# Kernel tuning notes

Hardware: AMD Instinct MI355X
Metric: run time of the kernel (lower is better)

Reference implementation:

```python
import jax, jax.numpy as jnp
import numpy as np

L_MAX = 3          # max output angular momentum (L_max in the module)
N_L_IN = 4         # input l = 0..3, all with sigma = +1
Q = 16             # q_max per input block
N_SAMPLES = 4000   # number of atomic environments (samples)


def _combos():
    # Mirrors CGIteration.initialize: for each (l1,s1=1) x (l2,s2=1) pair,
    # emit L in |l1-l2|..min(l1+l2, L_max), S = (-1)^(l1+l2+L).
    out = []
    for l1 in range(N_L_IN):
        for l2 in range(N_L_IN):
            for L in range(abs(l1 - l2), min(l1 + l2, L_MAX) + 1):
                out.append((l1, l2, L, (-1) ** (l1 + l2 + L)))
    return out


def setup_inputs() -> dict:
    key = jax.random.key(0)
    ks = jax.random.split(key, 9)
    inp = {}
    for l in range(N_L_IN):
        inp[f"x1_l{l}"] = jax.random.normal(ks[l], (N_SAMPLES, 2 * l + 1, Q), dtype=jnp.float32)
        inp[f"x2_l{l}"] = jax.random.normal(ks[4 + l], (N_SAMPLES, 2 * l + 1, Q), dtype=jnp.float32)
    # Padded Clebsch-Gordan coefficient table: cg_coeffs[l1, l2, L, m1, m2, M]
    # (slices [:2l1+1, :2l2+1, :2L+1] are used; padding is ignored).
    inp["cg_coeffs"] = jax.random.normal(
        ks[8], (N_L_IN, N_L_IN, L_MAX + 1, 2 * N_L_IN - 1, 2 * N_L_IN - 1, 2 * L_MAX + 1),
        dtype=jnp.float32)
    return inp


def _forward(x1, x2, cg_coeffs):
    # One species; per-(L,S) output block lists, then concat along properties.
    blocks = {}
    for l1, l2, L, S in _combos():
        C = cg_coeffs[l1, l2, L, :2 * l1 + 1, :2 * l2 + 1, :2 * L + 1]  # [m1, m2, M]
        # cg.combine with 'full' selected_features == full cartesian (q1, q2)
        # outer product: out[n, M, q1, q2] = sum_{m1,m2} C[m1,m2,M] x1[n,m1,q1] x2[n,m2,q2]
        b = jnp.einsum('nip,njq,ijM->nMpq', x1[l1], x2[l2], C)
        b = b.reshape(b.shape[0], 2 * L + 1, -1)  # [n, 2L+1, q1*q2]
        blocks.setdefault((L, S), []).append(b)
    outs = []
    for key in sorted(blocks.keys()):
        v = jnp.concatenate(blocks[key], axis=-1)      # cat along 'mixed' properties
        outs.append(v.reshape(v.shape[0], -1))         # flatten (m, properties)
    return jnp.concatenate(outs, axis=-1)              # [n, 39936]


def reference(x1_l0, x1_l1, x1_l2, x1_l3, x2_l0, x2_l1, x2_l2, x2_l3, cg_coeffs):
    x1 = [x1_l0, x1_l1, x1_l2, x1_l3]
    x2 = [x2_l0, x2_l1, x2_l2, x2_l3]
    return _forward(x1, x2, cg_coeffs)
```

## Files before the change

### kernel.cpp

```cpp
#include <hip/hip_runtime.h>


namespace {

constexpr int NC = 34;

struct CInfo { int l1, l2, L, pbase, outbase, mstride; };
struct CTable { CInfo c[NC]; int packed_total; int outsize; };

constexpr CTable build_table() {
  CTable t{};
  int nb[4][2] = {};
  for (int l1 = 0; l1 < 4; ++l1)
    for (int l2 = 0; l2 < 4; ++l2) {
      int lo = l1 > l2 ? l1 - l2 : l2 - l1;
      int hi = (l1 + l2 < 3) ? l1 + l2 : 3;
      for (int L = lo; L <= hi; ++L)
        nb[L][((l1 + l2 + L) & 1) ? 0 : 1]++;
    }
  int keyoff[4][2] = {};
  int off = 0;
  for (int L = 0; L < 4; ++L)
    for (int s = 0; s < 2; ++s) {
      keyoff[L][s] = off;
      off += (2 * L + 1) * 256 * nb[L][s];
    }
  t.outsize = off;
  int blk[4][2] = {};
  int idx = 0, pb = 0;
  for (int l1 = 0; l1 < 4; ++l1)
    for (int l2 = 0; l2 < 4; ++l2) {
      int lo = l1 > l2 ? l1 - l2 : l2 - l1;
      int hi = (l1 + l2 < 3) ? l1 + l2 : 3;
      for (int L = lo; L <= hi; ++L) {
        int s = ((l1 + l2 + L) & 1) ? 0 : 1;
        pb = (pb + 15) & ~15;
        t.c[idx].l1 = l1; t.c[idx].l2 = l2; t.c[idx].L = L;
        t.c[idx].pbase = pb;
        t.c[idx].outbase = keyoff[L][s] + blk[L][s] * 256;
        t.c[idx].mstride = 256 * nb[L][s];
        blk[L][s]++;
        pb += (2 * l1 + 1) * (2 * l2 + 1) * (2 * L + 1);
        ++idx;
      }
    }
  t.packed_total = pb;
  return t;
}

constexpr CTable CTAB = build_table();
static_assert(CTAB.outsize == 39936, "output layout mismatch");
static_assert(CTAB.packed_total <= 4096, "packed cg exceeds 16KB");

template <int CI>
__device__ __forceinline__ void pack_combo(const float* __restrict__ cg,
                                           float* __restrict__ cgp, int tid) {
  if constexpr (CI < NC) {
    constexpr CInfo c = CTAB.c[CI];
    constexpr int D2 = 2 * c.l2 + 1, DL = 2 * c.L + 1;
    constexpr int SZ = (2 * c.l1 + 1) * D2 * DL;
    for (int tt = tid; tt < SZ; tt += 256) {
      int M = tt % DL, ij = tt / DL;
      int j = ij % D2, i = ij / D2;
      cgp[c.pbase + tt] =
          cg[((((c.l1 * 4 + c.l2) * 4 + c.L) * 7 + i) * 7 + j) * 7 + M];
    }
    pack_combo<CI + 1>(cg, cgp, tid);
  }
}

__global__ void pack_cg_kernel(const float* __restrict__ cg,
                               float* __restrict__ cgp) {
  pack_combo<0>(cg, cgp, (int)threadIdx.x);
}

template <int CI>
__device__ __forceinline__ void run_combos(const float* __restrict__ cgp,
                                           const float (&x1r)[16],
                                           const float (&x2r)[16],
                                           float* __restrict__ outn) {
  if constexpr (CI < NC) {
    constexpr CInfo c = CTAB.c[CI];
    constexpr int D1 = 2 * c.l1 + 1, D2 = 2 * c.l2 + 1, DL = 2 * c.L + 1;
    constexpr int R1 = c.l1 * c.l1, R2 = c.l2 * c.l2;
    float acc[DL];
#pragma unroll
    for (int M = 0; M < DL; ++M) acc[M] = 0.f;
#pragma unroll
    for (int i = 0; i < D1; ++i) {
#pragma unroll
      for (int j = 0; j < D2; ++j) {
        const float ab = x1r[R1 + i] * x2r[R2 + j];
#pragma unroll
        for (int M = 0; M < DL; ++M)
          acc[M] = fmaf(cgp[c.pbase + (i * D2 + j) * DL + M], ab, acc[M]);
      }
    }
#pragma unroll
    for (int M = 0; M < DL; ++M)
      outn[c.outbase + M * c.mstride] = acc[M];
    run_combos<CI + 1>(cgp, x1r, x2r, outn);
  }
}

__global__ __launch_bounds__(256) void cg_main(
    const float* __restrict__ x1_0, const float* __restrict__ x2_0,
    const float* __restrict__ x1_1, const float* __restrict__ x2_1,
    const float* __restrict__ x1_2, const float* __restrict__ x2_2,
    const float* __restrict__ x1_3, const float* __restrict__ x2_3,
    const float* __restrict__ cgp_, float* __restrict__ out) {
  const float* cgp = (const float*)__builtin_assume_aligned(cgp_, 256);
  __shared__ float x1s[16][16];
  __shared__ float x2s[16][16];
  const int tid = (int)threadIdx.x;
  const int n = (int)blockIdx.x;
  const int r = tid >> 4, col = tid & 15;
  const float* s1; const float* s2; int ri;
  if (r < 1)      { s1 = x1_0 + n * 16;  s2 = x2_0 + n * 16;  ri = r; }
  else if (r < 4) { s1 = x1_1 + n * 48;  s2 = x2_1 + n * 48;  ri = r - 1; }
  else if (r < 9) { s1 = x1_2 + n * 80;  s2 = x2_2 + n * 80;  ri = r - 4; }
  else            { s1 = x1_3 + n * 112; s2 = x2_3 + n * 112; ri = r - 9; }
  x1s[r][col] = s1[ri * 16 + col];
  x2s[r][col] = s2[ri * 16 + col];
  __syncthreads();
  float x1r[16], x2r[16];
#pragma unroll
  for (int k = 0; k < 16; ++k) {
    x1r[k] = x1s[k][r];
    x2r[k] = x2s[k][col];
  }
  float* outn = out + (size_t)n * (size_t)CTAB.outsize + tid;
  run_combos<0>(cgp, x1r, x2r, outn);
}

}

extern "C" void kernel_launch(void* const* d_in, const int* in_sizes, int n_in,
                              void* d_out, int out_size, void* d_ws,
                              size_t ws_size, hipStream_t stream) {
  const float* x1[4];
  const float* x2[4];
  if (in_sizes[1] == in_sizes[0]) {
    for (int l = 0; l < 4; ++l) {
      x1[l] = (const float*)d_in[2 * l];
      x2[l] = (const float*)d_in[2 * l + 1];
    }
  } else {
    for (int l = 0; l < 4; ++l) {
      x1[l] = (const float*)d_in[l];
      x2[l] = (const float*)d_in[4 + l];
    }
  }
  const float* cg = (const float*)d_in[8];
  float* out = (float*)d_out;
  float* cgp = (float*)d_ws;

  const int n = in_sizes[0] / 16;

  pack_cg_kernel<<<1, 256, 0, stream>>>(cg, cgp);
  cg_main<<<n, 256, 0, stream>>>(x1[0], x2[0], x1[1], x2[1], x1[2], x2[2],
                                 x1[3], x2[3], cgp, out);
}
```

Before: 168.8 us.

## Stage output segments in LDS and write them with vectorized nontemporal stores

```diff
diff --git a/kernel.cpp b/kernel.cpp
--- a/kernel.cpp
+++ b/kernel.cpp
@@ -3,30 +3,39 @@
 
 namespace {
 
+typedef float f32x4 __attribute__((ext_vector_type(4)));
+
 constexpr int NC = 34;
-
-struct CInfo { int l1, l2, L, pbase, outbase, mstride; };
-struct CTable { CInfo c[NC]; int packed_total; int outsize; };
-
-constexpr CTable build_table() {
-  CTable t{};
-  int nb[4][2] = {};
+constexpr int SEGF = 6144;
+
+struct CInfo { int l1, l2, L, s, pbase, blk, nb, segbase; };
+struct PInfo { int kidx, M0, M1, base, floats; };
+struct Tables {
+  CInfo c[NC];
+  PInfo p[16];
+  int np;
+  int packed_total;
+  int outsize;
+};
+
+constexpr Tables build() {
+  Tables t{};
+  int nb[8] = {};
   for (int l1 = 0; l1 < 4; ++l1)
     for (int l2 = 0; l2 < 4; ++l2) {
       int lo = l1 > l2 ? l1 - l2 : l2 - l1;
       int hi = (l1 + l2 < 3) ? l1 + l2 : 3;
       for (int L = lo; L <= hi; ++L)
-        nb[L][((l1 + l2 + L) & 1) ? 0 : 1]++;
-    }
-  int keyoff[4][2] = {};
+        nb[L * 2 + (((l1 + l2 + L) & 1) ? 0 : 1)]++;
+    }
+  int segbase[8] = {};
   int off = 0;
-  for (int L = 0; L < 4; ++L)
-    for (int s = 0; s < 2; ++s) {
-      keyoff[L][s] = off;
-      off += (2 * L + 1) * 256 * nb[L][s];
-    }
+  for (int k = 0; k < 8; ++k) {
+    segbase[k] = off;
+    off += (2 * (k >> 1) + 1) * 256 * nb[k];
+  }
   t.outsize = off;
-  int blk[4][2] = {};
+  int blk[8] = {};
   int idx = 0, pb = 0;
   for (int l1 = 0; l1 < 4; ++l1)
     for (int l2 = 0; l2 < 4; ++l2) {
@@ -34,29 +43,49 @@
       int hi = (l1 + l2 < 3) ? l1 + l2 : 3;
       for (int L = lo; L <= hi; ++L) {
         int s = ((l1 + l2 + L) & 1) ? 0 : 1;
+        int k = L * 2 + s;
         pb = (pb + 15) & ~15;
-        t.c[idx].l1 = l1; t.c[idx].l2 = l2; t.c[idx].L = L;
+        t.c[idx].l1 = l1; t.c[idx].l2 = l2; t.c[idx].L = L; t.c[idx].s = s;
         t.c[idx].pbase = pb;
-        t.c[idx].outbase = keyoff[L][s] + blk[L][s] * 256;
-        t.c[idx].mstride = 256 * nb[L][s];
-        blk[L][s]++;
+        t.c[idx].blk = blk[k];
+        t.c[idx].nb = nb[k];
+        t.c[idx].segbase = segbase[k];
+        blk[k]++;
         pb += (2 * l1 + 1) * (2 * l2 + 1) * (2 * L + 1);
         ++idx;
       }
     }
   t.packed_total = pb;
+  int np = 0;
+  for (int k = 0; k < 8; ++k) {
+    if (nb[k] == 0) continue;
+    int DL = 2 * (k >> 1) + 1;
+    int sr = nb[k] * 256;
+    int maxsr = SEGF / sr;
+    int M0 = 0;
+    while (M0 < DL) {
+      int M1 = M0 + maxsr < DL ? M0 + maxsr : DL;
+      t.p[np].kidx = k; t.p[np].M0 = M0; t.p[np].M1 = M1;
+      t.p[np].base = segbase[k] + M0 * sr;
+      t.p[np].floats = (M1 - M0) * sr;
+      ++np;
+      M0 = M1;
+    }
+  }
+  t.np = np;
   return t;
 }
 
-constexpr CTable CTAB = build_table();
-static_assert(CTAB.outsize == 39936, "output layout mismatch");
-static_assert(CTAB.packed_total <= 4096, "packed cg exceeds 16KB");
+constexpr Tables TAB = build();
+static_assert(TAB.outsize == 39936, "output layout mismatch");
+static_assert(TAB.packed_total <= 4096, "packed cg exceeds 16KB");
+static_assert(TAB.np <= 16, "too many passes");
 
 template <int CI>
 __device__ __forceinline__ void pack_combo(const float* __restrict__ cg,
                                            float* __restrict__ cgp, int tid) {
   if constexpr (CI < NC) {
-    constexpr CInfo c = CTAB.c[CI];
+    constexpr CInfo c = TAB.c[CI];
     constexpr int D2 = 2 * c.l2 + 1, DL = 2 * c.L + 1;
     constexpr int SZ = (2 * c.l1 + 1) * D2 * DL;
     for (int tt = tid; tt < SZ; tt += 256) {
@@ -74,32 +103,64 @@
   pack_combo<0>(cg, cgp, (int)threadIdx.x);
 }
 
-template <int CI>
-__device__ __forceinline__ void run_combos(const float* __restrict__ cgp,
+template <int PI, int CI>
+__device__ __forceinline__ void pass_combos(const float* __restrict__ cgp,
+                                            const float (&x1r)[16],
+                                            const float (&x2r)[16],
+                                            float* __restrict__ seg, int tid) {
+  if constexpr (CI < NC) {
+    constexpr PInfo P = TAB.p[PI];
+    constexpr CInfo c = TAB.c[CI];
+    if constexpr (c.L * 2 + c.s == P.kidx) {
+      constexpr int D1 = 2 * c.l1 + 1, D2 = 2 * c.l2 + 1, DL = 2 * c.L + 1;
+      constexpr int R1 = c.l1 * c.l1, R2 = c.l2 * c.l2;
+      constexpr int NA = P.M1 - P.M0;
+      float acc[NA];
+#pragma unroll
+      for (int m = 0; m < NA; ++m) acc[m] = 0.f;
+#pragma unroll
+      for (int i = 0; i < D1; ++i) {
+#pragma unroll
+        for (int j = 0; j < D2; ++j) {
+          const float ab = x1r[R1 + i] * x2r[R2 + j];
+#pragma unroll
+          for (int m = 0; m < NA; ++m)
+            acc[m] = fmaf(cgp[c.pbase + (i * D2 + j) * DL + P.M0 + m], ab,
+                          acc[m]);
+        }
+      }
+#pragma unroll
+      for (int m = 0; m < NA; ++m)
+        seg[m * (c.nb * 256) + c.blk * 256 + tid] = acc[m];
+    }
+    pass_combos<PI, CI + 1>(cgp, x1r, x2r, seg, tid);
+  }
+}
+
+template <int PI>
+__device__ __forceinline__ void run_passes(const float* __restrict__ cgp,
                                            const float (&x1r)[16],
                                            const float (&x2r)[16],
-                                           float* __restrict__ outn) {
-  if constexpr (CI < NC) {
-    constexpr CInfo c = CTAB.c[CI];
-    constexpr int D1 = 2 * c.l1 + 1, D2 = 2 * c.l2 + 1, DL = 2 * c.L + 1;
-    constexpr int R1 = c.l1 * c.l1, R2 = c.l2 * c.l2;
-    float acc[DL];
-#pragma unroll
-    for (int M = 0; M < DL; ++M) acc[M] = 0.f;
-#pragma unroll
-    for (int i = 0; i < D1; ++i) {
-#pragma unroll
-      for (int j = 0; j < D2; ++j) {
-        const float ab = x1r[R1 + i] * x2r[R2 + j];
-#pragma unroll
-        for (int M = 0; M < DL; ++M)
-          acc[M] = fmaf(cgp[c.pbase + (i * D2 + j) * DL + M], ab, acc[M]);
+                                           float* __restrict__ seg,
+                                           float* __restrict__ outn, int tid) {
+  if constexpr (PI < TAB.np) {
+    pass_combos<PI, 0>(cgp, x1r, x2r, seg, tid);
+    __syncthreads();
+    constexpr PInfo P = TAB.p[PI];
+    constexpr int NF4 = P.floats / 4;
+    const f32x4* sb = reinterpret_cast<const f32x4*>(seg);
+    f32x4* ob = reinterpret_cast<f32x4*>(outn + P.base);
+#pragma unroll
+    for (int k = 0; k < (NF4 + 255) / 256; ++k) {
+      const int idx = tid + 256 * k;
+      if constexpr ((NF4 & 255) == 0) {
+        __builtin_nontemporal_store(sb[idx], ob + idx);
+      } else {
+        if (idx < NF4) __builtin_nontemporal_store(sb[idx], ob + idx);
       }
     }
-#pragma unroll
-    for (int M = 0; M < DL; ++M)
-      outn[c.outbase + M * c.mstride] = acc[M];
-    run_combos<CI + 1>(cgp, x1r, x2r, outn);
+    __syncthreads();
+    run_passes<PI + 1>(cgp, x1r, x2r, seg, outn, tid);
   }
 }
 
@@ -112,6 +173,7 @@
   const float* cgp = (const float*)__builtin_assume_aligned(cgp_, 256);
   __shared__ float x1s[16][16];
   __shared__ float x2s[16][16];
+  __shared__ __align__(16) float seg[SEGF];
   const int tid = (int)threadIdx.x;
   const int n = (int)blockIdx.x;
   const int r = tid >> 4, col = tid & 15;
@@ -129,8 +191,8 @@
     x1r[k] = x1s[k][r];
     x2r[k] = x2s[k][col];
   }
-  float* outn = out + (size_t)n * (size_t)CTAB.outsize + tid;
-  run_combos<0>(cgp, x1r, x2r, outn);
+  float* outn = out + (size_t)n * (size_t)TAB.outsize;
+  run_passes<0>(cgp, x1r, x2r, seg, outn, tid);
 }
 
 }
```

Result: slower. 317.8 us (+88.2%).

## Split work per (L,S) key across blocks and stage output in LDS for vector stores

Applied to the files above, without the earlier changes.

```diff
diff --git a/kernel.cpp b/kernel.cpp
--- a/kernel.cpp
+++ b/kernel.cpp
@@ -3,30 +3,33 @@
 
 namespace {
 
+typedef float f32x4 __attribute__((ext_vector_type(4)));
+
 constexpr int NC = 34;
-
-struct CInfo { int l1, l2, L, pbase, outbase, mstride; };
-struct CTable { CInfo c[NC]; int packed_total; int outsize; };
-
-constexpr CTable build_table() {
-  CTable t{};
-  int nb[4][2] = {};
+constexpr int NKEY = 8;
+
+struct CInfo { int l1, l2, L, s, pbase, blk; };
+struct KInfo { int nb, segbase, segfloats; };
+struct Tables { CInfo c[NC]; KInfo k[NKEY]; int packed_total; int outsize; int segmax; };
+
+constexpr Tables build() {
+  Tables t{};
+  int nb[NKEY] = {};
   for (int l1 = 0; l1 < 4; ++l1)
     for (int l2 = 0; l2 < 4; ++l2) {
       int lo = l1 > l2 ? l1 - l2 : l2 - l1;
       int hi = (l1 + l2 < 3) ? l1 + l2 : 3;
       for (int L = lo; L <= hi; ++L)
-        nb[L][((l1 + l2 + L) & 1) ? 0 : 1]++;
-    }
-  int keyoff[4][2] = {};
+        nb[L * 2 + (((l1 + l2 + L) & 1) ? 0 : 1)]++;
+    }
+  int segbase[NKEY] = {};
   int off = 0;
-  for (int L = 0; L < 4; ++L)
-    for (int s = 0; s < 2; ++s) {
-      keyoff[L][s] = off;
-      off += (2 * L + 1) * 256 * nb[L][s];
-    }
+  for (int k = 0; k < NKEY; ++k) {
+    segbase[k] = off;
+    off += (2 * (k >> 1) + 1) * 256 * nb[k];
+  }
   t.outsize = off;
-  int blk[4][2] = {};
+  int blk[NKEY] = {};
   int idx = 0, pb = 0;
   for (int l1 = 0; l1 < 4; ++l1)
     for (int l2 = 0; l2 < 4; ++l2) {
@@ -34,29 +37,40 @@
       int hi = (l1 + l2 < 3) ? l1 + l2 : 3;
       for (int L = lo; L <= hi; ++L) {
         int s = ((l1 + l2 + L) & 1) ? 0 : 1;
+        int k = L * 2 + s;
         pb = (pb + 15) & ~15;
-        t.c[idx].l1 = l1; t.c[idx].l2 = l2; t.c[idx].L = L;
+        t.c[idx].l1 = l1; t.c[idx].l2 = l2; t.c[idx].L = L; t.c[idx].s = s;
         t.c[idx].pbase = pb;
-        t.c[idx].outbase = keyoff[L][s] + blk[L][s] * 256;
-        t.c[idx].mstride = 256 * nb[L][s];
-        blk[L][s]++;
+        t.c[idx].blk = blk[k];
+        blk[k]++;
         pb += (2 * l1 + 1) * (2 * l2 + 1) * (2 * L + 1);
         ++idx;
       }
     }
   t.packed_total = pb;
+  int mx = 0;
+  for (int k = 0; k < NKEY; ++k) {
+    t.k[k].nb = nb[k];
+    t.k[k].segbase = segbase[k];
+    t.k[k].segfloats = (2 * (k >> 1) + 1) * 256 * nb[k];
+    if (t.k[k].segfloats > mx) mx = t.k[k].segfloats;
+  }
+  t.segmax = mx;
   return t;
 }
 
-constexpr CTable CTAB = build_table();
-static_assert(CTAB.outsize == 39936, "output layout mismatch");
-static_assert(CTAB.packed_total <= 4096, "packed cg exceeds 16KB");
+constexpr Tables TAB = build();
+static_assert(TAB.outsize == 39936, "output layout mismatch");
+static_assert(TAB.packed_total <= 4096, "packed cg exceeds 16KB");
+static_assert(TAB.segmax == 10752, "unexpected max segment");
+static_assert(TAB.k[0].segfloats == 0, "key 0 (L=0,S=-1) should be empty");
+static_assert(TAB.k[1].segfloats == 1024, "key 1 (L=0,S=+1) should be 4 blocks");
 
 template <int CI>
 __device__ __forceinline__ void pack_combo(const float* __restrict__ cg,
                                            float* __restrict__ cgp, int tid) {
   if constexpr (CI < NC) {
-    constexpr CInfo c = CTAB.c[CI];
+    constexpr CInfo c = TAB.c[CI];
     constexpr int D2 = 2 * c.l2 + 1, DL = 2 * c.L + 1;
     constexpr int SZ = (2 * c.l1 + 1) * D2 * DL;
     for (int tt = tid; tt < SZ; tt += 256) {
@@ -74,32 +88,59 @@
   pack_combo<0>(cg, cgp, (int)threadIdx.x);
 }
 
-template <int CI>
-__device__ __forceinline__ void run_combos(const float* __restrict__ cgp,
+template <int K, int CI>
+__device__ __forceinline__ void key_combos(const float* __restrict__ cgp,
                                            const float (&x1r)[16],
                                            const float (&x2r)[16],
-                                           float* __restrict__ outn) {
+                                           float* __restrict__ seg, int tid) {
   if constexpr (CI < NC) {
-    constexpr CInfo c = CTAB.c[CI];
-    constexpr int D1 = 2 * c.l1 + 1, D2 = 2 * c.l2 + 1, DL = 2 * c.L + 1;
-    constexpr int R1 = c.l1 * c.l1, R2 = c.l2 * c.l2;
-    float acc[DL];
-#pragma unroll
-    for (int M = 0; M < DL; ++M) acc[M] = 0.f;
-#pragma unroll
-    for (int i = 0; i < D1; ++i) {
-#pragma unroll
-      for (int j = 0; j < D2; ++j) {
-        const float ab = x1r[R1 + i] * x2r[R2 + j];
-#pragma unroll
-        for (int M = 0; M < DL; ++M)
-          acc[M] = fmaf(cgp[c.pbase + (i * D2 + j) * DL + M], ab, acc[M]);
+    constexpr CInfo c = TAB.c[CI];
+    if constexpr (c.L * 2 + c.s == K) {
+      constexpr int D1 = 2 * c.l1 + 1, D2 = 2 * c.l2 + 1, DL = 2 * c.L + 1;
+      constexpr int R1 = c.l1 * c.l1, R2 = c.l2 * c.l2;
+      constexpr int NBC = TAB.k[K].nb * 256;
+      float acc[DL];
+#pragma unroll
+      for (int M = 0; M < DL; ++M) acc[M] = 0.f;
+#pragma unroll
+      for (int i = 0; i < D1; ++i) {
+#pragma unroll
+        for (int j = 0; j < D2; ++j) {
+          const float ab = x1r[R1 + i] * x2r[R2 + j];
+#pragma unroll
+          for (int M = 0; M < DL; ++M)
+            acc[M] = fmaf(cgp[c.pbase + (i * D2 + j) * DL + M], ab, acc[M]);
+        }
       }
-    }
-#pragma unroll
-    for (int M = 0; M < DL; ++M)
-      outn[c.outbase + M * c.mstride] = acc[M];
-    run_combos<CI + 1>(cgp, x1r, x2r, outn);
+#pragma unroll
+      for (int M = 0; M < DL; ++M)
+        seg[M * NBC + c.blk * 256 + tid] = acc[M];
+    }
+    key_combos<K, CI + 1>(cgp, x1r, x2r, seg, tid);
+  }
+}
+
+template <int K>
+__device__ __forceinline__ void do_key(const float* __restrict__ cgp,
+                                       const float (&x1r)[16],
+                                       const float (&x2r)[16],
+                                       float* __restrict__ seg,
+                                       float* __restrict__ outseg, int tid) {
+  if constexpr (TAB.k[K].segfloats > 0) {
+    key_combos<K, 0>(cgp, x1r, x2r, seg, tid);
+    __syncthreads();
+    constexpr int NF4 = TAB.k[K].segfloats / 4;
+    const f32x4* sb = reinterpret_cast<const f32x4*>(seg);
+    f32x4* ob = reinterpret_cast<f32x4*>(outseg);
+#pragma unroll
+    for (int k0 = 0; k0 < (NF4 + 255) / 256; ++k0) {
+      const int idx = tid + 256 * k0;
+      if constexpr ((NF4 & 255) == 0) {
+        ob[idx] = sb[idx];
+      } else {
+        if (idx < NF4) ob[idx] = sb[idx];
+      }
+    }
   }
 }
 
@@ -108,12 +149,17 @@
     const float* __restrict__ x1_1, const float* __restrict__ x2_1,
     const float* __restrict__ x1_2, const float* __restrict__ x2_2,
     const float* __restrict__ x1_3, const float* __restrict__ x2_3,
-    const float* __restrict__ cgp_, float* __restrict__ out) {
+    const float* __restrict__ cgp_, float* __restrict__ out, int nsamp) {
   const float* cgp = (const float*)__builtin_assume_aligned(cgp_, 256);
   __shared__ float x1s[16][16];
   __shared__ float x2s[16][16];
+  __shared__ __align__(16) float seg[TAB.segmax];
   const int tid = (int)threadIdx.x;
-  const int n = (int)blockIdx.x;
+  const int id = (int)blockIdx.x;
+  const int xcd = id & 7, g = id >> 3;
+  const int flat = xcd * nsamp + g;
+  const int n = flat >> 3;
+  const int key = flat & 7;
   const int r = tid >> 4, col = tid & 15;
   const float* s1; const float* s2; int ri;
   if (r < 1)      { s1 = x1_0 + n * 16;  s2 = x2_0 + n * 16;  ri = r; }
@@ -129,8 +175,17 @@
     x1r[k] = x1s[k][r];
     x2r[k] = x2s[k][col];
   }
-  float* outn = out + (size_t)n * (size_t)CTAB.outsize + tid;
-  run_combos<0>(cgp, x1r, x2r, outn);
+  float* outrow = out + (size_t)n * (size_t)TAB.outsize;
+  switch (key) {
+    case 0: do_key<0>(cgp, x1r, x2r, seg, outrow + TAB.k[0].segbase, tid); break;
+    case 1: do_key<1>(cgp, x1r, x2r, seg, outrow + TAB.k[1].segbase, tid); break;
+    case 2: do_key<2>(cgp, x1r, x2r, seg, outrow + TAB.k[2].segbase, tid); break;
+    case 3: do_key<3>(cgp, x1r, x2r, seg, outrow + TAB.k[3].segbase, tid); break;
+    case 4: do_key<4>(cgp, x1r, x2r, seg, outrow + TAB.k[4].segbase, tid); break;
+    case 5: do_key<5>(cgp, x1r, x2r, seg, outrow + TAB.k[5].segbase, tid); break;
+    case 6: do_key<6>(cgp, x1r, x2r, seg, outrow + TAB.k[6].segbase, tid); break;
+    case 7: do_key<7>(cgp, x1r, x2r, seg, outrow + TAB.k[7].segbase, tid); break;
+  }
 }
 
 }
@@ -158,6 +213,6 @@
   const int n = in_sizes[0] / 16;
 
   pack_cg_kernel<<<1, 256, 0, stream>>>(cg, cgp);
-  cg_main<<<n, 256, 0, stream>>>(x1[0], x2[0], x1[1], x2[1], x1[2], x2[2],
-                                 x1[3], x2[3], cgp, out);
-}
+  cg_main<<<8 * n, 256, 0, stream>>>(x1[0], x2[0], x1[1], x2[1], x1[2],
+                                     x2[2], x1[3], x2[3], cgp, out, n);
+}
```

New measurement: 233.5 us. 1.38x slower.

## Factor CG contraction into two stages with shared-memory intermediate

Applied to the files above, without the earlier changes.

```diff
diff --git a/kernel.cpp b/kernel.cpp
--- a/kernel.cpp
+++ b/kernel.cpp
@@ -3,10 +3,13 @@
 
 namespace {
 
+typedef float f32x4 __attribute__((ext_vector_type(4)));
+
 constexpr int NC = 34;
-
-struct CInfo { int l1, l2, L, pbase, outbase, mstride; };
-struct CTable { CInfo c[NC]; int packed_total; int outsize; };
+constexpr int TSTR = 1028;
+
+struct CInfo { int l1, l2, L, pbase2, outbase, mstride, tb, ofs; };
+struct CTable { CInfo c[NC]; int packed2; int outsize; int ttotal; };
 
 constexpr CTable build_table() {
   CTable t{};
@@ -27,79 +30,143 @@
     }
   t.outsize = off;
   int blk[4][2] = {};
-  int idx = 0, pb = 0;
+  int idx = 0, pb2 = 0, tb = 0, fill = 0;
   for (int l1 = 0; l1 < 4; ++l1)
     for (int l2 = 0; l2 < 4; ++l2) {
       int lo = l1 > l2 ? l1 - l2 : l2 - l1;
       int hi = (l1 + l2 < 3) ? l1 + l2 : 3;
       for (int L = lo; L <= hi; ++L) {
         int s = ((l1 + l2 + L) & 1) ? 0 : 1;
-        pb = (pb + 15) & ~15;
+        int D1 = 2 * l1 + 1, D2 = 2 * l2 + 1, DL = 2 * L + 1;
+        int DP = (DL + 3) & ~3;
         t.c[idx].l1 = l1; t.c[idx].l2 = l2; t.c[idx].L = L;
-        t.c[idx].pbase = pb;
+        t.c[idx].pbase2 = pb2;
         t.c[idx].outbase = keyoff[L][s] + blk[L][s] * 256;
         t.c[idx].mstride = 256 * nb[L][s];
+        t.c[idx].tb = tb;
+        if (fill + D1 * 16 > 256) fill = 0;
+        t.c[idx].ofs = fill;
+        fill += D1 * 16;
         blk[L][s]++;
-        pb += (2 * l1 + 1) * (2 * l2 + 1) * (2 * L + 1);
+        pb2 += D1 * D2 * DP;
+        tb += D1 * DP;
         ++idx;
       }
     }
-  t.packed_total = pb;
+  t.packed2 = pb2;
+  t.ttotal = tb;
   return t;
 }
 
 constexpr CTable CTAB = build_table();
 static_assert(CTAB.outsize == 39936, "output layout mismatch");
-static_assert(CTAB.packed_total <= 4096, "packed cg exceeds 16KB");
+static_assert(CTAB.ttotal == TSTR, "T stride mismatch");
+static_assert(CTAB.packed2 <= 8192, "packed cg exceeds 32KB");
 
 template <int CI>
 __device__ __forceinline__ void pack_combo(const float* __restrict__ cg,
-                                           float* __restrict__ cgp, int tid) {
+                                           float* __restrict__ cgp2, int tid) {
   if constexpr (CI < NC) {
     constexpr CInfo c = CTAB.c[CI];
     constexpr int D2 = 2 * c.l2 + 1, DL = 2 * c.L + 1;
+    constexpr int DP = (DL + 3) & ~3;
     constexpr int SZ = (2 * c.l1 + 1) * D2 * DL;
     for (int tt = tid; tt < SZ; tt += 256) {
       int M = tt % DL, ij = tt / DL;
       int j = ij % D2, i = ij / D2;
-      cgp[c.pbase + tt] =
+      cgp2[c.pbase2 + ij * DP + M] =
           cg[((((c.l1 * 4 + c.l2) * 4 + c.L) * 7 + i) * 7 + j) * 7 + M];
     }
-    pack_combo<CI + 1>(cg, cgp, tid);
+    pack_combo<CI + 1>(cg, cgp2, tid);
   }
 }
 
 __global__ void pack_cg_kernel(const float* __restrict__ cg,
-                               float* __restrict__ cgp) {
-  pack_combo<0>(cg, cgp, (int)threadIdx.x);
+                               float* __restrict__ cgp2) {
+  for (int i = (int)threadIdx.x; i < CTAB.packed2; i += 256) cgp2[i] = 0.f;
+  __syncthreads();
+  pack_combo<0>(cg, cgp2, (int)threadIdx.x);
 }
 
 template <int CI>
-__device__ __forceinline__ void run_combos(const float* __restrict__ cgp,
-                                           const float (&x1r)[16],
-                                           const float (&x2r)[16],
-                                           float* __restrict__ outn) {
+__device__ __forceinline__ void step1(const float* __restrict__ cgp2,
+                                      const float* __restrict__ x2s,
+                                      float* __restrict__ T, int tid) {
   if constexpr (CI < NC) {
     constexpr CInfo c = CTAB.c[CI];
     constexpr int D1 = 2 * c.l1 + 1, D2 = 2 * c.l2 + 1, DL = 2 * c.L + 1;
-    constexpr int R1 = c.l1 * c.l1, R2 = c.l2 * c.l2;
+    constexpr int DP = (DL + 3) & ~3;
+    constexpr int R2 = c.l2 * c.l2;
+    const unsigned d = (unsigned)(tid - c.ofs) & 255u;
+    if (d < (unsigned)(D1 * 16)) {
+      const int i = (int)(d >> 4), q = (int)(d & 15u);
+      float acc[DL];
+#pragma unroll
+      for (int M = 0; M < DL; ++M) acc[M] = 0.f;
+#pragma unroll
+      for (int j = 0; j < D2; ++j) {
+        const float xv = x2s[(R2 + j) * 16 + q];
+        const f32x4 k0 = *reinterpret_cast<const f32x4*>(
+            cgp2 + c.pbase2 + (i * D2 + j) * DP);
+        f32x4 k1{};
+        if constexpr (DP == 8)
+          k1 = *reinterpret_cast<const f32x4*>(cgp2 + c.pbase2 +
+                                               (i * D2 + j) * DP + 4);
+#pragma unroll
+        for (int M = 0; M < DL; ++M) {
+          const float cc = (M < 4) ? k0[M & 3] : k1[M & 3];
+          acc[M] = fmaf(cc, xv, acc[M]);
+        }
+      }
+      float* tp = T + q * TSTR + c.tb + i * DP;
+      f32x4 w0;
+      w0[0] = acc[0];
+      w0[1] = (DL > 1) ? acc[1 < DL ? 1 : 0] : 0.f;
+      w0[2] = (DL > 2) ? acc[2 < DL ? 2 : 0] : 0.f;
+      w0[3] = (DL > 3) ? acc[3 < DL ? 3 : 0] : 0.f;
+      *reinterpret_cast<f32x4*>(tp) = w0;
+      if constexpr (DP == 8) {
+        f32x4 w1;
+        w1[0] = acc[4 < DL ? 4 : 0];
+        w1[1] = (DL > 5) ? acc[5 < DL ? 5 : 0] : 0.f;
+        w1[2] = (DL > 6) ? acc[6 < DL ? 6 : 0] : 0.f;
+        w1[3] = 0.f;
+        *reinterpret_cast<f32x4*>(tp + 4) = w1;
+      }
+    }
+    step1<CI + 1>(cgp2, x2s, T, tid);
+  }
+}
+
+template <int CI>
+__device__ __forceinline__ void step2(const float* __restrict__ Tq,
+                                      const float (&x1r)[16],
+                                      float* __restrict__ outn) {
+  if constexpr (CI < NC) {
+    constexpr CInfo c = CTAB.c[CI];
+    constexpr int D1 = 2 * c.l1 + 1, DL = 2 * c.L + 1;
+    constexpr int DP = (DL + 3) & ~3;
+    constexpr int R1 = c.l1 * c.l1;
     float acc[DL];
 #pragma unroll
     for (int M = 0; M < DL; ++M) acc[M] = 0.f;
 #pragma unroll
     for (int i = 0; i < D1; ++i) {
-#pragma unroll
-      for (int j = 0; j < D2; ++j) {
-        const float ab = x1r[R1 + i] * x2r[R2 + j];
-#pragma unroll
-        for (int M = 0; M < DL; ++M)
-          acc[M] = fmaf(cgp[c.pbase + (i * D2 + j) * DL + M], ab, acc[M]);
+      const f32x4 t0 = *reinterpret_cast<const f32x4*>(Tq + c.tb + i * DP);
+      f32x4 t1{};
+      if constexpr (DP == 8)
+        t1 = *reinterpret_cast<const f32x4*>(Tq + c.tb + i * DP + 4);
+      const float a = x1r[R1 + i];
+#pragma unroll
+      for (int M = 0; M < DL; ++M) {
+        const float tv = (M < 4) ? t0[M & 3] : t1[M & 3];
+        acc[M] = fmaf(a, tv, acc[M]);
       }
     }
 #pragma unroll
     for (int M = 0; M < DL; ++M)
       outn[c.outbase + M * c.mstride] = acc[M];
-    run_combos<CI + 1>(cgp, x1r, x2r, outn);
+    step2<CI + 1>(Tq, x1r, outn);
   }
 }
 
@@ -108,29 +175,33 @@
     const float* __restrict__ x1_1, const float* __restrict__ x2_1,
     const float* __restrict__ x1_2, const float* __restrict__ x2_2,
     const float* __restrict__ x1_3, const float* __restrict__ x2_3,
-    const float* __restrict__ cgp_, float* __restrict__ out) {
-  const float* cgp = (const float*)__builtin_assume_aligned(cgp_, 256);
-  __shared__ float x1s[16][16];
-  __shared__ float x2s[16][16];
+    const float* __restrict__ cgp2_, float* __restrict__ out) {
+  const float* cgp2 = (const float*)__builtin_assume_aligned(cgp2_, 256);
+  __shared__ __align__(16) float lds[512 + 16 * TSTR];
+  float* x1s = lds;
+  float* x2s = lds + 256;
+  float* T = lds + 512;
   const int tid = (int)threadIdx.x;
   const int n = (int)blockIdx.x;
   const int r = tid >> 4, col = tid & 15;
-  const float* s1; const float* s2; int ri;
-  if (r < 1)      { s1 = x1_0 + n * 16;  s2 = x2_0 + n * 16;  ri = r; }
-  else if (r < 4) { s1 = x1_1 + n * 48;  s2 = x2_1 + n * 48;  ri = r - 1; }
-  else if (r < 9) { s1 = x1_2 + n * 80;  s2 = x2_2 + n * 80;  ri = r - 4; }
-  else            { s1 = x1_3 + n * 112; s2 = x2_3 + n * 112; ri = r - 9; }
-  x1s[r][col] = s1[ri * 16 + col];
-  x2s[r][col] = s2[ri * 16 + col];
+  {
+    const float* s1; const float* s2; int ri;
+    if (r < 1)      { s1 = x1_0 + n * 16;  s2 = x2_0 + n * 16;  ri = r; }
+    else if (r < 4) { s1 = x1_1 + n * 48;  s2 = x2_1 + n * 48;  ri = r - 1; }
+    else if (r < 9) { s1 = x1_2 + n * 80;  s2 = x2_2 + n * 80;  ri = r - 4; }
+    else            { s1 = x1_3 + n * 112; s2 = x2_3 + n * 112; ri = r - 9; }
+    x1s[r * 16 + col] = s1[ri * 16 + col];
+    x2s[r * 16 + col] = s2[ri * 16 + col];
+  }
   __syncthreads();
-  float x1r[16], x2r[16];
-#pragma unroll
-  for (int k = 0; k < 16; ++k) {
-    x1r[k] = x1s[k][r];
-    x2r[k] = x2s[k][col];
-  }
+  step1<0>(cgp2, x2s, T, tid);
+  __syncthreads();
+  float x1r[16];
+#pragma unroll
+  for (int k = 0; k < 16; ++k) x1r[k] = x1s[k * 16 + r];
+  const float* Tq = T + col * TSTR;
   float* outn = out + (size_t)n * (size_t)CTAB.outsize + tid;
-  run_combos<0>(cgp, x1r, x2r, outn);
+  step2<0>(Tq, x1r, outn);
 }
 
 }
@@ -153,11 +224,11 @@
   }
   const float* cg = (const float*)d_in[8];
   float* out = (float*)d_out;
-  float* cgp = (float*)d_ws;
+  float* cgp2 = (float*)d_ws;
 
   const int n = in_sizes[0] / 16;
 
-  pack_cg_kernel<<<1, 256, 0, stream>>>(cg, cgp);
+  pack_cg_kernel<<<1, 256, 0, stream>>>(cg, cgp2);
   cg_main<<<n, 256, 0, stream>>>(x1[0], x2[0], x1[1], x2[1], x1[2], x2[2],
-                                 x1[3], x2[3], cgp, out);
-}
+                                 x1[3], x2[3], cgp2, out);
+}
```

After: 176.3 us. 1.04x slower.
